# Kernel optimization log

Measured on AMD Instinct MI355X. Metric: run time of the kernel, lower is better.

Reference implementation:

```python
import jax, jax.numpy as jnp
import numpy as np
from itertools import combinations

B, F, K, V = 1024, 39, 16, 200000  # batch, fields, embed dim, vocab
EPS = 1e-3  # tf.layers.batch_normalization default epsilon


def setup_inputs() -> dict:
    key = jax.random.key(0)
    ks = jax.random.split(key, 6)
    pairs = np.array(list(combinations(range(F), 2)), dtype=np.int32)   # [741, 2]
    trips = np.array(list(combinations(range(F), 3)), dtype=np.int32)   # [9139, 3]
    P, T = pairs.shape[0], trips.shape[0]
    return {
        "feats": jax.random.randint(ks[0], (B, F), 0, V, dtype=jnp.int32),
        "w": jax.random.normal(ks[1], (V,), dtype=jnp.float32) * 0.01,
        "v": jax.random.normal(ks[2], (V, K), dtype=jnp.float32) * 0.01,
        "b": jnp.zeros((1,), dtype=jnp.float32),
        "gamma2": jnp.ones((P,), dtype=jnp.float32),
        "beta2": jnp.zeros((P,), dtype=jnp.float32),
        "gw2": jax.random.uniform(ks[3], (P,), minval=0.599, maxval=0.601, dtype=jnp.float32),
        "gamma3": jnp.ones((T,), dtype=jnp.float32),
        "beta3": jnp.zeros((T,), dtype=jnp.float32),
        "gw3": jax.random.uniform(ks[4], (T,), minval=0.599, maxval=0.601, dtype=jnp.float32),
        "rows": jnp.asarray(pairs[:, 1]),   # second element of each pair
        "cols": jnp.asarray(pairs[:, 0]),   # first element of each pair
        "i1": jnp.asarray(trips[:, 0]),
        "i2": jnp.asarray(trips[:, 1]),
        "i3": jnp.asarray(trips[:, 2]),
    }


def _batchnorm(x, gamma, beta):
    # training-mode BN over batch axis; x: [B, P]
    m = jnp.mean(x, axis=0)
    var = jnp.mean(jnp.square(x - m), axis=0)
    return (x - m) * jax.lax.rsqrt(var + EPS) * gamma + beta


def reference(feats, w, v, b, gamma2, beta2, gw2, gamma3, beta3, gw3,
              rows, cols, i1, i2, i3):
    xw = w[feats]            # [B, F]  first-order weights
    xv = v[feats]            # [B, F, K] embeddings
    l = jnp.sum(xw, axis=1)  # linear term [B]

    # second-order: gather pair embeddings, multiply, reduce over K
    level2 = jnp.sum(xv[:, rows, :] * xv[:, cols, :], axis=-1)  # [B, P]
    level2 = _batchnorm(level2, gamma2, beta2) * gw2            # soft mask
    fm_out = jnp.sum(level2, axis=-1)                           # [B]

    # third-order: gather triple embeddings
    level3 = jnp.sum(xv[:, i1, :] * xv[:, i2, :] * xv[:, i3, :], axis=-1)  # [B, T]
    level3 = _batchnorm(level3, gamma3, beta3) * gw3
    fm_out2 = jnp.sum(level3, axis=-1)                          # [B]

    logits = l + fm_out + fm_out2 + b[0]                        # [B]
    return logits
```

## Files before the change

kernel.cpp:

```cpp
#include <hip/hip_runtime.h>
#include <hip/hip_fp16.h>
#include <math.h>

#define B_ 1024
#define F_ 39
#define K_ 16
#define P_ 741
#define T_ 9139
#define NC_ 9880
#define EPS_ 1e-3f
#define YSTR 24
#define ESTR 40
#define LS2 9920
#define NSPLIT 32

typedef _Float16 half2v __attribute__((ext_vector_type(2)));

__device__ __forceinline__ float hdot2(unsigned a, unsigned b, float acc) {
    half2v ha = __builtin_bit_cast(half2v, a);
    half2v hb = __builtin_bit_cast(half2v, b);
#if __has_builtin(__builtin_amdgcn_fdot2)
    return __builtin_amdgcn_fdot2(ha, hb, acc, false);
#else
    return acc + (float)ha.x * (float)hb.x + (float)ha.y * (float)hb.y;
#endif
}
__device__ __forceinline__ float f16f(unsigned short h) {
    return __half2float(__builtin_bit_cast(__half, h));
}

__global__ __launch_bounds__(256) void prep_k(const int* __restrict__ rows,
                                              const int* __restrict__ cols,
                                              const int* __restrict__ i1,
                                              const int* __restrict__ i2,
                                              const int* __restrict__ i3,
                                              unsigned* __restrict__ pidx,
                                              float* __restrict__ Cacc) {
    int c = blockIdx.x * 256 + threadIdx.x;
    if (c >= NC_) return;
    if (c == 0) Cacc[0] = 0.f;
    unsigned pk;
    if (c < P_) {
        pk = (unsigned)(cols[c] * ESTR) | ((unsigned)(rows[c] * ESTR) << 11);
    } else {
        int t = c - P_;
        int a = i1[t], b = i2[t], cc = i3[t];
        int p = a * (2 * F_ - 1 - a) / 2 + (b - a - 1);
        pk = (unsigned)(p * YSTR) | ((unsigned)(cc * ESTR) << 15);
    }
    pidx[c] = pk;
}

__global__ __launch_bounds__(512) void levels_k(const int* __restrict__ feats,
                                                const float* __restrict__ v,
                                                const unsigned* __restrict__ pidx,
                                                unsigned short* __restrict__ levels) {
    int b = blockIdx.x;
    int tid = threadIdx.x;
    __shared__ int tok[F_];
    __shared__ __attribute__((aligned(16))) unsigned short emb2[F_ * ESTR];
    __shared__ __attribute__((aligned(16))) unsigned short Y2[P_ * YSTR];

    unsigned short* lrow = levels + (size_t)b * LS2;

    unsigned pk_p0 = (tid < P_) ? pidx[tid] : 0u;
    unsigned pk_p1 = (tid + 512 < P_) ? pidx[tid + 512] : 0u;
    unsigned pkt[18];
#pragma unroll
    for (int i = 0; i < 18; ++i) {
        int t = i * 512 + tid;
        pkt[i] = (t < T_) ? pidx[P_ + t] : 0u;
    }

    if (tid < F_) tok[tid] = feats[b * F_ + tid];
    __syncthreads();
    for (int idx = tid; idx < F_ * K_; idx += 512) {
        int f = idx >> 4, k = idx & 15;
        emb2[f * ESTR + k] = __builtin_bit_cast(unsigned short,
                                 __float2half(v[(size_t)tok[f] * K_ + k]));
    }
    __syncthreads();

#pragma unroll 1
    for (int pp = 0; pp < 2; ++pp) {
        int p = pp * 512 + tid;
        if (p < P_) {
            unsigned pk = pp == 0 ? pk_p0 : pk_p1;
            int o1 = (int)(pk & 2047u);
            int o2 = (int)((pk >> 11) & 2047u);
            uint4 ua0 = *(const uint4*)&emb2[o1];
            uint4 ua1 = *(const uint4*)&emb2[o1 + 8];
            uint4 uc0 = *(const uint4*)&emb2[o2];
            uint4 uc1 = *(const uint4*)&emb2[o2 + 8];
            float s = 0.f;
            uint4 y0, y1;
#define PKMUL(dst, a, c) {                                                    \
            half2v _a = __builtin_bit_cast(half2v, a);                        \
            half2v _c = __builtin_bit_cast(half2v, c);                        \
            half2v _y = _a * _c;                                              \
            dst = __builtin_bit_cast(unsigned, _y);                           \
            s = hdot2(a, c, s); }
            PKMUL(y0.x, ua0.x, uc0.x); PKMUL(y0.y, ua0.y, uc0.y);
            PKMUL(y0.z, ua0.z, uc0.z); PKMUL(y0.w, ua0.w, uc0.w);
            PKMUL(y1.x, ua1.x, uc1.x); PKMUL(y1.y, ua1.y, uc1.y);
            PKMUL(y1.z, ua1.z, uc1.z); PKMUL(y1.w, ua1.w, uc1.w);
#undef PKMUL
            *(uint4*)&Y2[p * YSTR] = y0;
            *(uint4*)&Y2[p * YSTR + 8] = y1;
            lrow[p] = __builtin_bit_cast(unsigned short, __float2half(s));
        }
    }
    __syncthreads();

#pragma unroll 3
    for (int i = 0; i < 18; ++i) {
        int t = i * 512 + tid;
        if (t < T_) {
            unsigned pk = pkt[i];
            int yb = (int)(pk & 32767u);
            int o3 = (int)(pk >> 15);
            uint4 uy0 = *(const uint4*)&Y2[yb];
            uint4 uy1 = *(const uint4*)&Y2[yb + 8];
            uint4 ue0 = *(const uint4*)&emb2[o3];
            uint4 ue1 = *(const uint4*)&emb2[o3 + 8];
            float s = 0.f;
            s = hdot2(uy0.x, ue0.x, s); s = hdot2(uy0.y, ue0.y, s);
            s = hdot2(uy0.z, ue0.z, s); s = hdot2(uy0.w, ue0.w, s);
            s = hdot2(uy1.x, ue1.x, s); s = hdot2(uy1.y, ue1.y, s);
            s = hdot2(uy1.z, ue1.z, s);
            s = hdot2(uy1.w, ue1.w, s);
            lrow[P_ + t] = __builtin_bit_cast(unsigned short, __float2half(s));
        }
    }
}

__global__ __launch_bounds__(256) void stats2_k(const unsigned short* __restrict__ levels,
                                                float* __restrict__ psum,
                                                float* __restrict__ psumsq) {
    int col2 = blockIdx.x * 256 + threadIdx.x;
    if (col2 >= NC_ / 2) return;
    int sy = blockIdx.y;
    const unsigned* p = (const unsigned*)(levels + (size_t)(sy * (B_ / NSPLIT)) * LS2)
                        + col2;
    float s0 = 0.f, s1 = 0.f, q0 = 0.f, q1 = 0.f;
    float s2 = 0.f, s3 = 0.f, q2 = 0.f, q3 = 0.f;
#pragma unroll
    for (int r = 0; r < B_ / NSPLIT; r += 4) {
        unsigned u0 = p[(size_t)(r + 0) * (LS2 / 2)];
        unsigned u1 = p[(size_t)(r + 1) * (LS2 / 2)];
        unsigned u2 = p[(size_t)(r + 2) * (LS2 / 2)];
        unsigned u3 = p[(size_t)(r + 3) * (LS2 / 2)];
        float2 f0 = __half22float2(__builtin_bit_cast(__half2, u0));
        float2 f1 = __half22float2(__builtin_bit_cast(__half2, u1));
        float2 f2 = __half22float2(__builtin_bit_cast(__half2, u2));
        float2 f3 = __half22float2(__builtin_bit_cast(__half2, u3));
        s0 += f0.x; q0 += f0.x * f0.x; s1 += f0.y; q1 += f0.y * f0.y;
        s2 += f1.x; q2 += f1.x * f1.x; s3 += f1.y; q3 += f1.y * f1.y;
        s0 += f2.x; q0 += f2.x * f2.x; s1 += f2.y; q1 += f2.y * f2.y;
        s2 += f3.x; q2 += f3.x * f3.x; s3 += f3.y; q3 += f3.y * f3.y;
    }
    float2 sv; sv.x = s0 + s2; sv.y = s1 + s3;
    float2 qv; qv.x = q0 + q2; qv.y = q1 + q3;
    ((float2*)psum)[(size_t)sy * (NC_ / 2) + col2]   = sv;
    ((float2*)psumsq)[(size_t)sy * (NC_ / 2) + col2] = qv;
}

__global__ __launch_bounds__(256) void finalize_k(const float* __restrict__ psum,
                                                  const float* __restrict__ psumsq,
                                                  const float* __restrict__ gamma2,
                                                  const float* __restrict__ beta2,
                                                  const float* __restrict__ gw2,
                                                  const float* __restrict__ gamma3,
                                                  const float* __restrict__ beta3,
                                                  const float* __restrict__ gw3,
                                                  float* __restrict__ scale,
                                                  float* __restrict__ Cacc) {
    int col = blockIdx.x * 256 + threadIdx.x;
    float c = 0.f;
    if (col < NC_) {
        float s1 = 0.f, s2 = 0.f;
#pragma unroll 8
        for (int sy = 0; sy < NSPLIT; ++sy) {
            s1 += psum[(size_t)sy * NC_ + col];
            s2 += psumsq[(size_t)sy * NC_ + col];
        }
        float mean = s1 * (1.0f / B_);
        float var  = s2 * (1.0f / B_) - mean * mean;
        float inv  = 1.0f / sqrtf(var + EPS_);
        float g, be, gw;
        if (col < P_) {
            g = gamma2[col]; be = beta2[col]; gw = gw2[col];
        } else {
            int t = col - P_;
            g = gamma3[t]; be = beta3[t]; gw = gw3[t];
        }
        scale[col] = gw * g * inv;
        c = gw * (be - g * inv * mean);
    }
    __shared__ float red[256];
    red[threadIdx.x] = c;
    __syncthreads();
    for (int s = 128; s > 0; s >>= 1) {
        if (threadIdx.x < s) red[threadIdx.x] += red[threadIdx.x + s];
        __syncthreads();
    }
    if (threadIdx.x == 0) atomicAdd(Cacc, red[0]);
}

__global__ __launch_bounds__(256) void out_k(const unsigned short* __restrict__ levels,
                                             const float* __restrict__ scale,
                                             const int* __restrict__ feats,
                                             const float* __restrict__ w,
                                             const float* __restrict__ Cacc,
                                             const float* __restrict__ bias,
                                             float* __restrict__ out) {
    int b = blockIdx.x, tid = threadIdx.x;
    const uint4* lv = (const uint4*)(levels + (size_t)b * LS2);
    float acc = 0.f;
    for (int idx = tid; idx < 1235; idx += 256) {
        uint4 u = lv[idx];
        float4 sa = *(const float4*)&scale[idx * 8];
        float4 sb = *(const float4*)&scale[idx * 8 + 4];
        float2 f0 = __half22float2(__builtin_bit_cast(__half2, u.x));
        float2 f1 = __half22float2(__builtin_bit_cast(__half2, u.y));
        float2 f2 = __half22float2(__builtin_bit_cast(__half2, u.z));
        float2 f3 = __half22float2(__builtin_bit_cast(__half2, u.w));
        acc += sa.x * f0.x + sa.y * f0.y + sa.z * f1.x + sa.w * f1.y;
        acc += sb.x * f2.x + sb.y * f2.y + sb.z * f3.x + sb.w * f3.y;
    }
    if (tid < F_) acc += w[feats[b * F_ + tid]];
    __shared__ float red[256];
    red[tid] = acc;
    __syncthreads();
    for (int s = 128; s > 0; s >>= 1) {
        if (tid < s) red[tid] += red[tid + s];
        __syncthreads();
    }
    if (tid == 0) out[b] = red[0] + Cacc[0] + bias[0];
}

extern "C" void kernel_launch(void* const* d_in, const int* in_sizes, int n_in,
                              void* d_out, int out_size, void* d_ws, size_t ws_size,
                              hipStream_t stream) {
    const int*   feats  = (const int*)d_in[0];
    const float* w      = (const float*)d_in[1];
    const float* v      = (const float*)d_in[2];
    const float* bias   = (const float*)d_in[3];
    const float* gamma2 = (const float*)d_in[4];
    const float* beta2  = (const float*)d_in[5];
    const float* gw2    = (const float*)d_in[6];
    const float* gamma3 = (const float*)d_in[7];
    const float* beta3  = (const float*)d_in[8];
    const float* gw3    = (const float*)d_in[9];
    const int*   rows   = (const int*)d_in[10];
    const int*   cols   = (const int*)d_in[11];
    const int*   i1     = (const int*)d_in[12];
    const int*   i2     = (const int*)d_in[13];
    const int*   i3     = (const int*)d_in[14];
    float*       out    = (float*)d_out;
    float*       ws     = (float*)d_ws;

    float*          scale    = ws;
    float*          psum     = ws + 9880;
    float*          psumsq   = ws + 326040;
    float*          Cacc     = ws + 642200;
    unsigned*       pidx     = (unsigned*)(ws + 642304);
    unsigned short* levels   = (unsigned short*)(ws + 652224);

    prep_k<<<(NC_ + 255) / 256, 256, 0, stream>>>(rows, cols, i1, i2, i3, pidx, Cacc);
    levels_k<<<B_, 512, 0, stream>>>(feats, v, pidx, levels);
    stats2_k<<<dim3((NC_ / 2 + 255) / 256, NSPLIT), 256, 0, stream>>>(levels, psum, psumsq);
    finalize_k<<<(NC_ + 255) / 256, 256, 0, stream>>>(psum, psumsq,
                                                      gamma2, beta2, gw2,
                                                      gamma3, beta3, gw3, scale, Cacc);
    out_k<<<B_, 256, 0, stream>>>(levels, scale, feats, w, Cacc, bias, out);
}
```

Measured before the change: 125.1 us.

## Fuse five kernels into one cooperative persistent kernel with grid syncs

Replaces the prep, levels, stats, finalize and output kernels with a single cooperative kernel of 512 blocks. Each block handles two batch rows, and grid.sync separates the phases. The index-packing prep kernel is dropped; pair and triple indices are now read and computed inline from global memory on every row. This removes four launch gaps and inter-kernel drain, at the cost of grid-wide barriers, reduced per-row parallelism, and extra index loads in the hot loop.

Measured after the change: 316.1 us. 153% more time.

```diff
diff --git a/kernel.cpp b/kernel.cpp
--- a/kernel.cpp
+++ b/kernel.cpp
@@ -1,4 +1,5 @@
 #include <hip/hip_runtime.h>
+#include <hip/hip_cooperative_groups.h>
 #include <hip/hip_fp16.h>
 #include <math.h>
 
@@ -13,6 +14,10 @@
 #define ESTR 40
 #define LS2 9920
 #define NSPLIT 32
+#define NBLK 512
+#define NTHR 512
+
+namespace cg = cooperative_groups;
 
 typedef _Float16 half2v __attribute__((ext_vector_type(2)));
 
@@ -25,218 +30,193 @@
     return acc + (float)ha.x * (float)hb.x + (float)ha.y * (float)hb.y;
 #endif
 }
-__device__ __forceinline__ float f16f(unsigned short h) {
-    return __half2float(__builtin_bit_cast(__half, h));
-}
-
-__global__ __launch_bounds__(256) void prep_k(const int* __restrict__ rows,
-                                              const int* __restrict__ cols,
-                                              const int* __restrict__ i1,
-                                              const int* __restrict__ i2,
-                                              const int* __restrict__ i3,
-                                              unsigned* __restrict__ pidx,
-                                              float* __restrict__ Cacc) {
-    int c = blockIdx.x * 256 + threadIdx.x;
-    if (c >= NC_) return;
-    if (c == 0) Cacc[0] = 0.f;
-    unsigned pk;
-    if (c < P_) {
-        pk = (unsigned)(cols[c] * ESTR) | ((unsigned)(rows[c] * ESTR) << 11);
-    } else {
-        int t = c - P_;
-        int a = i1[t], b = i2[t], cc = i3[t];
-        int p = a * (2 * F_ - 1 - a) / 2 + (b - a - 1);
-        pk = (unsigned)(p * YSTR) | ((unsigned)(cc * ESTR) << 15);
-    }
-    pidx[c] = pk;
-}
-
-__global__ __launch_bounds__(512) void levels_k(const int* __restrict__ feats,
-                                                const float* __restrict__ v,
-                                                const unsigned* __restrict__ pidx,
-                                                unsigned short* __restrict__ levels) {
-    int b = blockIdx.x;
-    int tid = threadIdx.x;
+
+__global__ __launch_bounds__(NTHR, 4) void fused_k(
+        const int* __restrict__ feats, const float* __restrict__ w,
+        const float* __restrict__ v, const float* __restrict__ bias,
+        const float* __restrict__ gamma2, const float* __restrict__ beta2,
+        const float* __restrict__ gw2, const float* __restrict__ gamma3,
+        const float* __restrict__ beta3, const float* __restrict__ gw3,
+        const int* __restrict__ rows, const int* __restrict__ cols,
+        const int* __restrict__ i1, const int* __restrict__ i2,
+        const int* __restrict__ i3, float* __restrict__ scale,
+        float* __restrict__ psum, float* __restrict__ psumsq,
+        float* __restrict__ Cacc, unsigned short* __restrict__ levels,
+        float* __restrict__ out) {
+    cg::grid_group grid = cg::this_grid();
+    int blk = blockIdx.x, tid = threadIdx.x;
     __shared__ int tok[F_];
     __shared__ __attribute__((aligned(16))) unsigned short emb2[F_ * ESTR];
     __shared__ __attribute__((aligned(16))) unsigned short Y2[P_ * YSTR];
-
-    unsigned short* lrow = levels + (size_t)b * LS2;
-
-    unsigned pk_p0 = (tid < P_) ? pidx[tid] : 0u;
-    unsigned pk_p1 = (tid + 512 < P_) ? pidx[tid + 512] : 0u;
-    unsigned pkt[18];
+    __shared__ float red[NTHR];
+
+    if (blk == 0 && tid == 0) Cacc[0] = 0.f;
+
+    for (int rr = 0; rr < 2; ++rr) {
+        int b = blk * 2 + rr;
+        unsigned short* lrow = levels + (size_t)b * LS2;
+        if (tid < F_) tok[tid] = feats[b * F_ + tid];
+        __syncthreads();
+        for (int idx = tid; idx < F_ * K_; idx += NTHR) {
+            int f = idx >> 4, k = idx & 15;
+            emb2[f * ESTR + k] = __builtin_bit_cast(unsigned short,
+                                     __float2half(v[(size_t)tok[f] * K_ + k]));
+        }
+        __syncthreads();
+
+#pragma unroll 1
+        for (int pp = 0; pp < 2; ++pp) {
+            int p = pp * NTHR + tid;
+            if (p < P_) {
+                int o1 = cols[p] * ESTR;
+                int o2 = rows[p] * ESTR;
+                uint4 ua0 = *(const uint4*)&emb2[o1];
+                uint4 ua1 = *(const uint4*)&emb2[o1 + 8];
+                uint4 uc0 = *(const uint4*)&emb2[o2];
+                uint4 uc1 = *(const uint4*)&emb2[o2 + 8];
+                float s = 0.f;
+                uint4 y0, y1;
+#define PKMUL(dst, a, c) {                                                    \
+                half2v _a = __builtin_bit_cast(half2v, a);                    \
+                half2v _c = __builtin_bit_cast(half2v, c);                    \
+                half2v _y = _a * _c;                                          \
+                dst = __builtin_bit_cast(unsigned, _y);                       \
+                s = hdot2(a, c, s); }
+                PKMUL(y0.x, ua0.x, uc0.x); PKMUL(y0.y, ua0.y, uc0.y);
+                PKMUL(y0.z, ua0.z, uc0.z); PKMUL(y0.w, ua0.w, uc0.w);
+                PKMUL(y1.x, ua1.x, uc1.x); PKMUL(y1.y, ua1.y, uc1.y);
+                PKMUL(y1.z, ua1.z, uc1.z); PKMUL(y1.w, ua1.w, uc1.w);
+#undef PKMUL
+                *(uint4*)&Y2[p * YSTR] = y0;
+                *(uint4*)&Y2[p * YSTR + 8] = y1;
+                lrow[p] = __builtin_bit_cast(unsigned short, __float2half(s));
+            }
+        }
+        __syncthreads();
+
+#pragma unroll 3
+        for (int i = 0; i < 18; ++i) {
+            int t = i * NTHR + tid;
+            if (t < T_) {
+                int a = i1[t], bb = i2[t], c3 = i3[t];
+                int p = a * (2 * F_ - 1 - a) / 2 + (bb - a - 1);
+                int yb = p * YSTR;
+                int o3 = c3 * ESTR;
+                uint4 uy0 = *(const uint4*)&Y2[yb];
+                uint4 uy1 = *(const uint4*)&Y2[yb + 8];
+                uint4 ue0 = *(const uint4*)&emb2[o3];
+                uint4 ue1 = *(const uint4*)&emb2[o3 + 8];
+                float s = 0.f;
+                s = hdot2(uy0.x, ue0.x, s); s = hdot2(uy0.y, ue0.y, s);
+                s = hdot2(uy0.z, ue0.z, s); s = hdot2(uy0.w, ue0.w, s);
+                s = hdot2(uy1.x, ue1.x, s); s = hdot2(uy1.y, ue1.y, s);
+                s = hdot2(uy1.z, ue1.z, s); s = hdot2(uy1.w, ue1.w, s);
+                lrow[P_ + t] = __builtin_bit_cast(unsigned short, __float2half(s));
+            }
+        }
+        __syncthreads();
+    }
+    grid.sync();
+
+    {
+        int gid = blk * NTHR + tid;
+        if (gid < NSPLIT * (NC_ / 2)) {
+            int col2 = gid % (NC_ / 2);
+            int sy   = gid / (NC_ / 2);
+            const unsigned* p = (const unsigned*)levels
+                              + (size_t)(sy * (B_ / NSPLIT)) * (LS2 / 2) + col2;
+            float s0 = 0.f, s1 = 0.f, q0 = 0.f, q1 = 0.f;
+            float s2 = 0.f, s3 = 0.f, q2 = 0.f, q3 = 0.f;
 #pragma unroll
-    for (int i = 0; i < 18; ++i) {
-        int t = i * 512 + tid;
-        pkt[i] = (t < T_) ? pidx[P_ + t] : 0u;
-    }
-
-    if (tid < F_) tok[tid] = feats[b * F_ + tid];
-    __syncthreads();
-    for (int idx = tid; idx < F_ * K_; idx += 512) {
-        int f = idx >> 4, k = idx & 15;
-        emb2[f * ESTR + k] = __builtin_bit_cast(unsigned short,
-                                 __float2half(v[(size_t)tok[f] * K_ + k]));
-    }
-    __syncthreads();
-
-#pragma unroll 1
-    for (int pp = 0; pp < 2; ++pp) {
-        int p = pp * 512 + tid;
-        if (p < P_) {
-            unsigned pk = pp == 0 ? pk_p0 : pk_p1;
-            int o1 = (int)(pk & 2047u);
-            int o2 = (int)((pk >> 11) & 2047u);
-            uint4 ua0 = *(const uint4*)&emb2[o1];
-            uint4 ua1 = *(const uint4*)&emb2[o1 + 8];
-            uint4 uc0 = *(const uint4*)&emb2[o2];
-            uint4 uc1 = *(const uint4*)&emb2[o2 + 8];
-            float s = 0.f;
-            uint4 y0, y1;
-#define PKMUL(dst, a, c) {                                                    \
-            half2v _a = __builtin_bit_cast(half2v, a);                        \
-            half2v _c = __builtin_bit_cast(half2v, c);                        \
-            half2v _y = _a * _c;                                              \
-            dst = __builtin_bit_cast(unsigned, _y);                           \
-            s = hdot2(a, c, s); }
-            PKMUL(y0.x, ua0.x, uc0.x); PKMUL(y0.y, ua0.y, uc0.y);
-            PKMUL(y0.z, ua0.z, uc0.z); PKMUL(y0.w, ua0.w, uc0.w);
-            PKMUL(y1.x, ua1.x, uc1.x); PKMUL(y1.y, ua1.y, uc1.y);
-            PKMUL(y1.z, ua1.z, uc1.z); PKMUL(y1.w, ua1.w, uc1.w);
-#undef PKMUL
-            *(uint4*)&Y2[p * YSTR] = y0;
-            *(uint4*)&Y2[p * YSTR + 8] = y1;
-            lrow[p] = __builtin_bit_cast(unsigned short, __float2half(s));
-        }
-    }
-    __syncthreads();
-
-#pragma unroll 3
-    for (int i = 0; i < 18; ++i) {
-        int t = i * 512 + tid;
-        if (t < T_) {
-            unsigned pk = pkt[i];
-            int yb = (int)(pk & 32767u);
-            int o3 = (int)(pk >> 15);
-            uint4 uy0 = *(const uint4*)&Y2[yb];
-            uint4 uy1 = *(const uint4*)&Y2[yb + 8];
-            uint4 ue0 = *(const uint4*)&emb2[o3];
-            uint4 ue1 = *(const uint4*)&emb2[o3 + 8];
-            float s = 0.f;
-            s = hdot2(uy0.x, ue0.x, s); s = hdot2(uy0.y, ue0.y, s);
-            s = hdot2(uy0.z, ue0.z, s); s = hdot2(uy0.w, ue0.w, s);
-            s = hdot2(uy1.x, ue1.x, s); s = hdot2(uy1.y, ue1.y, s);
-            s = hdot2(uy1.z, ue1.z, s);
-            s = hdot2(uy1.w, ue1.w, s);
-            lrow[P_ + t] = __builtin_bit_cast(unsigned short, __float2half(s));
-        }
-    }
-}
-
-__global__ __launch_bounds__(256) void stats2_k(const unsigned short* __restrict__ levels,
-                                                float* __restrict__ psum,
-                                                float* __restrict__ psumsq) {
-    int col2 = blockIdx.x * 256 + threadIdx.x;
-    if (col2 >= NC_ / 2) return;
-    int sy = blockIdx.y;
-    const unsigned* p = (const unsigned*)(levels + (size_t)(sy * (B_ / NSPLIT)) * LS2)
-                        + col2;
-    float s0 = 0.f, s1 = 0.f, q0 = 0.f, q1 = 0.f;
-    float s2 = 0.f, s3 = 0.f, q2 = 0.f, q3 = 0.f;
+            for (int r = 0; r < B_ / NSPLIT; r += 4) {
+                unsigned u0 = p[(size_t)(r + 0) * (LS2 / 2)];
+                unsigned u1 = p[(size_t)(r + 1) * (LS2 / 2)];
+                unsigned u2 = p[(size_t)(r + 2) * (LS2 / 2)];
+                unsigned u3 = p[(size_t)(r + 3) * (LS2 / 2)];
+                float2 f0 = __half22float2(__builtin_bit_cast(__half2, u0));
+                float2 f1 = __half22float2(__builtin_bit_cast(__half2, u1));
+                float2 f2 = __half22float2(__builtin_bit_cast(__half2, u2));
+                float2 f3 = __half22float2(__builtin_bit_cast(__half2, u3));
+                s0 += f0.x; q0 += f0.x * f0.x; s1 += f0.y; q1 += f0.y * f0.y;
+                s2 += f1.x; q2 += f1.x * f1.x; s3 += f1.y; q3 += f1.y * f1.y;
+                s0 += f2.x; q0 += f2.x * f2.x; s1 += f2.y; q1 += f2.y * f2.y;
+                s2 += f3.x; q2 += f3.x * f3.x; s3 += f3.y; q3 += f3.y * f3.y;
+            }
+            float2 sv; sv.x = s0 + s2; sv.y = s1 + s3;
+            float2 qv; qv.x = q0 + q2; qv.y = q1 + q3;
+            ((float2*)psum)[(size_t)sy * (NC_ / 2) + col2]   = sv;
+            ((float2*)psumsq)[(size_t)sy * (NC_ / 2) + col2] = qv;
+        }
+    }
+    grid.sync();
+
+    {
+        int col = blk * NTHR + tid;
+        if (blk * NTHR < NC_) {
+            float c = 0.f;
+            if (col < NC_) {
+                float s1 = 0.f, s2 = 0.f;
+#pragma unroll 8
+                for (int sy = 0; sy < NSPLIT; ++sy) {
+                    s1 += psum[(size_t)sy * NC_ + col];
+                    s2 += psumsq[(size_t)sy * NC_ + col];
+                }
+                float mean = s1 * (1.0f / B_);
+                float var  = s2 * (1.0f / B_) - mean * mean;
+                float inv  = 1.0f / sqrtf(var + EPS_);
+                float g, be, gw;
+                if (col < P_) {
+                    g = gamma2[col]; be = beta2[col]; gw = gw2[col];
+                } else {
+                    int t = col - P_;
+                    g = gamma3[t]; be = beta3[t]; gw = gw3[t];
+                }
+                scale[col] = gw * g * inv;
+                c = gw * (be - g * inv * mean);
+            }
+            red[tid] = c;
+            __syncthreads();
+            for (int s = 256; s > 0; s >>= 1) {
+                if (tid < s) red[tid] += red[tid + s];
+                __syncthreads();
+            }
+            if (tid == 0) atomicAdd(Cacc, red[0]);
+        }
+    }
+    grid.sync();
+
+    {
+        float Cv = Cacc[0] + bias[0];
+        for (int rr = 0; rr < 2; ++rr) {
+            int b = blk * 2 + rr;
+            const uint4* lv = (const uint4*)(levels + (size_t)b * LS2);
+            float acc = 0.f;
 #pragma unroll
-    for (int r = 0; r < B_ / NSPLIT; r += 4) {
-        unsigned u0 = p[(size_t)(r + 0) * (LS2 / 2)];
-        unsigned u1 = p[(size_t)(r + 1) * (LS2 / 2)];
-        unsigned u2 = p[(size_t)(r + 2) * (LS2 / 2)];
-        unsigned u3 = p[(size_t)(r + 3) * (LS2 / 2)];
-        float2 f0 = __half22float2(__builtin_bit_cast(__half2, u0));
-        float2 f1 = __half22float2(__builtin_bit_cast(__half2, u1));
-        float2 f2 = __half22float2(__builtin_bit_cast(__half2, u2));
-        float2 f3 = __half22float2(__builtin_bit_cast(__half2, u3));
-        s0 += f0.x; q0 += f0.x * f0.x; s1 += f0.y; q1 += f0.y * f0.y;
-        s2 += f1.x; q2 += f1.x * f1.x; s3 += f1.y; q3 += f1.y * f1.y;
-        s0 += f2.x; q0 += f2.x * f2.x; s1 += f2.y; q1 += f2.y * f2.y;
-        s2 += f3.x; q2 += f3.x * f3.x; s3 += f3.y; q3 += f3.y * f3.y;
-    }
-    float2 sv; sv.x = s0 + s2; sv.y = s1 + s3;
-    float2 qv; qv.x = q0 + q2; qv.y = q1 + q3;
-    ((float2*)psum)[(size_t)sy * (NC_ / 2) + col2]   = sv;
-    ((float2*)psumsq)[(size_t)sy * (NC_ / 2) + col2] = qv;
-}
-
-__global__ __launch_bounds__(256) void finalize_k(const float* __restrict__ psum,
-                                                  const float* __restrict__ psumsq,
-                                                  const float* __restrict__ gamma2,
-                                                  const float* __restrict__ beta2,
-                                                  const float* __restrict__ gw2,
-                                                  const float* __restrict__ gamma3,
-                                                  const float* __restrict__ beta3,
-                                                  const float* __restrict__ gw3,
-                                                  float* __restrict__ scale,
-                                                  float* __restrict__ Cacc) {
-    int col = blockIdx.x * 256 + threadIdx.x;
-    float c = 0.f;
-    if (col < NC_) {
-        float s1 = 0.f, s2 = 0.f;
-#pragma unroll 8
-        for (int sy = 0; sy < NSPLIT; ++sy) {
-            s1 += psum[(size_t)sy * NC_ + col];
-            s2 += psumsq[(size_t)sy * NC_ + col];
-        }
-        float mean = s1 * (1.0f / B_);
-        float var  = s2 * (1.0f / B_) - mean * mean;
-        float inv  = 1.0f / sqrtf(var + EPS_);
-        float g, be, gw;
-        if (col < P_) {
-            g = gamma2[col]; be = beta2[col]; gw = gw2[col];
-        } else {
-            int t = col - P_;
-            g = gamma3[t]; be = beta3[t]; gw = gw3[t];
-        }
-        scale[col] = gw * g * inv;
-        c = gw * (be - g * inv * mean);
-    }
-    __shared__ float red[256];
-    red[threadIdx.x] = c;
-    __syncthreads();
-    for (int s = 128; s > 0; s >>= 1) {
-        if (threadIdx.x < s) red[threadIdx.x] += red[threadIdx.x + s];
-        __syncthreads();
-    }
-    if (threadIdx.x == 0) atomicAdd(Cacc, red[0]);
-}
-
-__global__ __launch_bounds__(256) void out_k(const unsigned short* __restrict__ levels,
-                                             const float* __restrict__ scale,
-                                             const int* __restrict__ feats,
-                                             const float* __restrict__ w,
-                                             const float* __restrict__ Cacc,
-                                             const float* __restrict__ bias,
-                                             float* __restrict__ out) {
-    int b = blockIdx.x, tid = threadIdx.x;
-    const uint4* lv = (const uint4*)(levels + (size_t)b * LS2);
-    float acc = 0.f;
-    for (int idx = tid; idx < 1235; idx += 256) {
-        uint4 u = lv[idx];
-        float4 sa = *(const float4*)&scale[idx * 8];
-        float4 sb = *(const float4*)&scale[idx * 8 + 4];
-        float2 f0 = __half22float2(__builtin_bit_cast(__half2, u.x));
-        float2 f1 = __half22float2(__builtin_bit_cast(__half2, u.y));
-        float2 f2 = __half22float2(__builtin_bit_cast(__half2, u.z));
-        float2 f3 = __half22float2(__builtin_bit_cast(__half2, u.w));
-        acc += sa.x * f0.x + sa.y * f0.y + sa.z * f1.x + sa.w * f1.y;
-        acc += sb.x * f2.x + sb.y * f2.y + sb.z * f3.x + sb.w * f3.y;
-    }
-    if (tid < F_) acc += w[feats[b * F_ + tid]];
-    __shared__ float red[256];
-    red[tid] = acc;
-    __syncthreads();
-    for (int s = 128; s > 0; s >>= 1) {
-        if (tid < s) red[tid] += red[tid + s];
-        __syncthreads();
-    }
-    if (tid == 0) out[b] = red[0] + Cacc[0] + bias[0];
+            for (int it = 0; it < 3; ++it) {
+                int idx = it * NTHR + tid;
+                if (idx < 1235) {
+                    uint4 u = lv[idx];
+                    float4 sa = *(const float4*)&scale[idx * 8];
+                    float4 sb = *(const float4*)&scale[idx * 8 + 4];
+                    float2 f0 = __half22float2(__builtin_bit_cast(__half2, u.x));
+                    float2 f1 = __half22float2(__builtin_bit_cast(__half2, u.y));
+                    float2 f2 = __half22float2(__builtin_bit_cast(__half2, u.z));
+                    float2 f3 = __half22float2(__builtin_bit_cast(__half2, u.w));
+                    acc += sa.x * f0.x + sa.y * f0.y + sa.z * f1.x + sa.w * f1.y;
+                    acc += sb.x * f2.x + sb.y * f2.y + sb.z * f3.x + sb.w * f3.y;
+                }
+            }
+            if (tid < F_) acc += w[feats[b * F_ + tid]];
+            __syncthreads();
+            red[tid] = acc;
+            __syncthreads();
+            for (int s = 256; s > 0; s >>= 1) {
+                if (tid < s) red[tid] += red[tid + s];
+                __syncthreads();
+            }
+            if (tid == 0) out[b] = red[0] + Cv;
+        }
+    }
 }
 
 extern "C" void kernel_launch(void* const* d_in, const int* in_sizes, int n_in,
@@ -260,18 +240,20 @@
     float*       out    = (float*)d_out;
     float*       ws     = (float*)d_ws;
 
-    float*          scale    = ws;
-    float*          psum     = ws + 9880;
-    float*          psumsq   = ws + 326040;
-    float*          Cacc     = ws + 642200;
-    unsigned*       pidx     = (unsigned*)(ws + 642304);
-    unsigned short* levels   = (unsigned short*)(ws + 652224);
-
-    prep_k<<<(NC_ + 255) / 256, 256, 0, stream>>>(rows, cols, i1, i2, i3, pidx, Cacc);
-    levels_k<<<B_, 512, 0, stream>>>(feats, v, pidx, levels);
-    stats2_k<<<dim3((NC_ / 2 + 255) / 256, NSPLIT), 256, 0, stream>>>(levels, psum, psumsq);
-    finalize_k<<<(NC_ + 255) / 256, 256, 0, stream>>>(psum, psumsq,
-                                                      gamma2, beta2, gw2,
-                                                      gamma3, beta3, gw3, scale, Cacc);
-    out_k<<<B_, 256, 0, stream>>>(levels, scale, feats, w, Cacc, bias, out);
+    float*          scale  = ws;
+    float*          psum   = ws + 9880;
+    float*          psumsq = ws + 326040;
+    float*          Cacc   = ws + 642200;
+    unsigned short* levels = (unsigned short*)(ws + 642304);
+
+    void* args[] = {
+        (void*)&feats, (void*)&w, (void*)&v, (void*)&bias,
+        (void*)&gamma2, (void*)&beta2, (void*)&gw2,
+        (void*)&gamma3, (void*)&beta3, (void*)&gw3,
+        (void*)&rows, (void*)&cols, (void*)&i1, (void*)&i2, (void*)&i3,
+        (void*)&scale, (void*)&psum, (void*)&psumsq, (void*)&Cacc,
+        (void*)&levels, (void*)&out
+    };
+    hipLaunchCooperativeKernel((const void*)fused_k, dim3(NBLK), dim3(NTHR),
+                               args, 0, stream);
 }
```
